# Kernel tuning notes

Hardware: AMD Instinct MI355X
Metric: run time of the kernel (lower is better)

The kernel has to match this reference:

```python
import jax, jax.numpy as jnp
import numpy as np

N, R, H, OUT = 512, 16, 16, 1
EPSILON = 1e-6
CUTOFF = 5.0  # ExpNormalSmearing cutoff_upper (cutoff_lower = 0)


def exp_normal_smearing(dist):
    # dist: (N, N, 1) -> (N, N, R); TorchMD-Net style ExpNormalSmearing
    start = jnp.exp(-CUTOFF)
    means = jnp.linspace(start, 1.0, R, dtype=dist.dtype)
    beta = (2.0 / R * (1.0 - start)) ** -2
    cutoff = 0.5 * (jnp.cos(dist * jnp.pi / CUTOFF) + 1.0) * (dist < CUTOFF)
    return cutoff * jnp.exp(-beta * (jnp.exp(-dist) - means) ** 2)


def setup_inputs() -> dict:
    key = jax.random.key(0)
    ks = jax.random.split(key, 9)
    s_in = 1.0 / np.sqrt(H * H)
    s_h = 1.0 / np.sqrt(H)
    return {
        "x": jax.random.normal(ks[0], (N, 3), jnp.float32) * 1.5,
        "W": jax.random.normal(ks[1], (2, N, R, H), jnp.float32) * 0.1,
        "W1": jax.random.normal(ks[2], (H, H * H), jnp.float32) * s_in,
        "b1": jax.random.normal(ks[3], (H,), jnp.float32) * 0.01,
        "W2": jax.random.normal(ks[4], (4 * R * H, H), jnp.float32) * s_h,
        "W3": jax.random.normal(ks[5], (H, H * H), jnp.float32) * s_in,
        "b3": jax.random.normal(ks[6], (H,), jnp.float32) * 0.01,
        "W4": jax.random.normal(ks[7], (OUT, H), jnp.float32) * s_h,
        "b4": jax.random.normal(ks[8], (OUT,), jnp.float32) * 0.01,
    }


def reference(x, W, W1, b1, W2, W3, b3, W4, b4):
    K, Q = W[0], W[1]                               # (N, R, H) each
    diff = x[:, None, :] - x[None, :, :]            # (N, N, 3)
    nsq = jnp.sum(diff * diff, axis=-1, keepdims=True) + EPSILON
    norm = jnp.sqrt(nsq)                            # (N, N, 1)
    diff = diff / nsq                               # note: divided by squared norm (faithful)
    sm = exp_normal_smearing(norm)                  # (N, N, R)
    basis = sm[..., None] * diff[..., None, :]      # (N, N, R, 3)

    bk = jnp.einsum('ijrb,jrc->icb', basis, K)      # (N, H, 3)
    bq = jnp.einsum('ijrb,jrc->icb', basis, Q)
    att = jnp.einsum('ihb,igb->ihg', bk, bq).reshape(N, H * H)
    att = jax.nn.silu(att @ W1.T + b1) @ W2.T       # (N, 4*R*H), second Linear bias-free

    left, right = att[:, : 2 * R * H], att[:, 2 * R * H:]
    pair = left[:, None, :] + right[None, :, :]     # (N, N, 2*R*H)
    K2 = pair[..., : R * H].reshape(N, N, R, H)
    Q2 = pair[..., R * H:].reshape(N, N, R, H)

    bk = jnp.einsum('ijrb,ijrc->icb', basis, K2)    # (N, H, 3)
    bq = jnp.einsum('ijrb,ijrc->icb', basis, Q2)
    att = jnp.einsum('ihb,igb->ihg', bk, bq).reshape(N, H * H)
    return jax.nn.silu(att @ W3.T + b3) @ W4.T + b4  # (N, OUT)
```

## Files before the change

### kernel.cpp

```cpp
#include <hip/hip_runtime.h>
#include <hip/hip_bf16.h>
#include <math.h>

#define NN 512

#define START 0.006737946999085467f
#define STEP  ((1.0f - START) * (1.0f/15.0f))
#define SB    (0.125f * (1.0f - START))
#define BETA  (1.0f/(SB*SB))
#define LOG2E 1.4426950408889634f
#define NB    (-(BETA)*LOG2E)


__global__ __launch_bounds__(256) void k1a(const float* __restrict__ x,
                                           const float* __restrict__ W,
                                           float* __restrict__ part1)
{
    const int ib = blockIdx.x & 127, jsH = blockIdx.x >> 7;
    const int i0 = ib * 4;
    const int tid = threadIdx.x;
    const int c = tid & 15, js = tid >> 4;
    const int lane = tid & 63, wv = tid >> 6;

    __shared__ float lG[1328];
    __shared__ float lP[256];
    __shared__ float s_part[4][16][26];

    const int gi = tid >> 6, gj = (tid >> 2) & 15, grq = tid & 3;
    const float gxi0 = x[(i0+gi)*3+0];
    const float gxi1 = x[(i0+gi)*3+1];
    const float gxi2 = x[(i0+gi)*3+2];

    float acc[24];
    #pragma unroll
    for (int v = 0; v < 24; ++v) acc[v] = 0.f;

    for (int jt = 0; jt < 4; ++jt) {
        const int jb = jsH*64 + jt*16;
        __syncthreads();

        {
            float d0 = gxi0 - x[(jb+gj)*3+0];
            float d1 = gxi1 - x[(jb+gj)*3+1];
            float d2 = gxi2 - x[(jb+gj)*3+2];
            float nsq = fmaf(d0,d0, fmaf(d1,d1, fmaf(d2,d2, 1e-6f)));
            float rs  = __builtin_amdgcn_rsqf(nsq);
            float nrm = nsq * rs;
            float inv = rs * rs;
            float cutv = 0.f;
            if (nrm < 5.0f) cutv = 0.5f*(__cosf(nrm*0.6283185307179586f)+1.0f);
            float en = exp2f(-LOG2E * nrm);
            if (grq == 0) {
                float4 dP; dP.x = d0*inv; dP.y = d1*inv; dP.z = d2*inv; dP.w = 0.f;
                *reinterpret_cast<float4*>(&lP[(gi*16+gj)*4]) = dP;
            }
            float4 g4;
            {
                float t0 = en - (START + STEP*(float)(grq*4+0));
                float t1 = en - (START + STEP*(float)(grq*4+1));
                float t2 = en - (START + STEP*(float)(grq*4+2));
                float t3 = en - (START + STEP*(float)(grq*4+3));
                g4.x = cutv * exp2f(NB*t0*t0);
                g4.y = cutv * exp2f(NB*t1*t1);
                g4.z = cutv * exp2f(NB*t2*t2);
                g4.w = cutv * exp2f(NB*t3*t3);
            }
            *reinterpret_cast<float4*>(&lG[gi*328 + gj*20 + grq*4]) = g4;
        }
        __syncthreads();

        const float* Kr = W + (size_t)(jb+js)*256 + c;
        const float* Qr = Kr + NN*256;
        float kk[16], qq[16];
        #pragma unroll
        for (int r = 0; r < 16; ++r) { kk[r] = Kr[r*16]; qq[r] = Qr[r*16]; }

        #pragma unroll
        for (int i = 0; i < 4; ++i) {
            const float4* gp = reinterpret_cast<const float4*>(&lG[i*328 + js*20]);
            float4 gA = gp[0], gB = gp[1], gC = gp[2], gD = gp[3];
            float tk = 0.f, tq = 0.f;
            tk = fmaf(gA.x,kk[ 0], tk); tq = fmaf(gA.x,qq[ 0], tq);
            tk = fmaf(gA.y,kk[ 1], tk); tq = fmaf(gA.y,qq[ 1], tq);
            tk = fmaf(gA.z,kk[ 2], tk); tq = fmaf(gA.z,qq[ 2], tq);
            tk = fmaf(gA.w,kk[ 3], tk); tq = fmaf(gA.w,qq[ 3], tq);
            tk = fmaf(gB.x,kk[ 4], tk); tq = fmaf(gB.x,qq[ 4], tq);
            tk = fmaf(gB.y,kk[ 5], tk); tq = fmaf(gB.y,qq[ 5], tq);
            tk = fmaf(gB.z,kk[ 6], tk); tq = fmaf(gB.z,qq[ 6], tq);
            tk = fmaf(gB.w,kk[ 7], tk); tq = fmaf(gB.w,qq[ 7], tq);
            tk = fmaf(gC.x,kk[ 8], tk); tq = fmaf(gC.x,qq[ 8], tq);
            tk = fmaf(gC.y,kk[ 9], tk); tq = fmaf(gC.y,qq[ 9], tq);
            tk = fmaf(gC.z,kk[10], tk); tq = fmaf(gC.z,qq[10], tq);
            tk = fmaf(gC.w,kk[11], tk); tq = fmaf(gC.w,qq[11], tq);
            tk = fmaf(gD.x,kk[12], tk); tq = fmaf(gD.x,qq[12], tq);
            tk = fmaf(gD.y,kk[13], tk); tq = fmaf(gD.y,qq[13], tq);
            tk = fmaf(gD.z,kk[14], tk); tq = fmaf(gD.z,qq[14], tq);
            tk = fmaf(gD.w,kk[15], tk); tq = fmaf(gD.w,qq[15], tq);
            float4 dd = *reinterpret_cast<const float4*>(&lP[(i*16+js)*4]);
            acc[i*6+0] = fmaf(tk, dd.x, acc[i*6+0]);
            acc[i*6+1] = fmaf(tk, dd.y, acc[i*6+1]);
            acc[i*6+2] = fmaf(tk, dd.z, acc[i*6+2]);
            acc[i*6+3] = fmaf(tq, dd.x, acc[i*6+3]);
            acc[i*6+4] = fmaf(tq, dd.y, acc[i*6+4]);
            acc[i*6+5] = fmaf(tq, dd.z, acc[i*6+5]);
        }
    }

    #pragma unroll
    for (int v = 0; v < 24; ++v) {
        float t = acc[v];
        t += __shfl_xor(t, 16);
        t += __shfl_xor(t, 32);
        if (lane < 16) s_part[wv][c][v] = t;
    }
    __syncthreads();

    for (int v = tid; v < 384; v += 256) {
        int i = v / 96, o = v - i*96;
        int kq = o / 48, rem = o - kq*48;
        int b = rem >> 4, c2 = rem & 15;
        int f = i*6 + kq*3 + b;
        float sum = s_part[0][c2][f] + s_part[1][c2][f]
                  + s_part[2][c2][f] + s_part[3][c2][f];
        part1[(i0+i)*768 + jsH*96 + o] = sum;
    }
}

__global__ __launch_bounds__(256) void k1b(const float* __restrict__ part1,
                                           const float* __restrict__ W1,
                                           const float* __restrict__ b1,
                                           const float* __restrict__ W2,
                                           float* __restrict__ att2)
{
    const int i = blockIdx.x;
    const int tid = threadIdx.x;
    __shared__ float s_bkq[96];
    __shared__ float s_att[256];
    __shared__ float s_z[16][16];
    __shared__ float s_a1[16];

    if (tid < 96) {
        const float* p = part1 + i*768 + tid;
        float s = 0.f;
        #pragma unroll
        for (int k = 0; k < 8; ++k) s += p[k*96];
        s_bkq[tid] = s;
    }
    __syncthreads();

    {
        int h = tid >> 4, g = tid & 15;
        s_att[tid] = s_bkq[     h]*s_bkq[48+     g]
                   + s_bkq[16 + h]*s_bkq[48+16 + g]
                   + s_bkq[32 + h]*s_bkq[48+32 + g];
    }
    __syncthreads();

    {
        int h = tid & 15, seg = tid >> 4;
        const float* w1 = W1 + h*256 + seg*16;
        const float* a  = s_att + seg*16;
        float p = 0.f;
        #pragma unroll
        for (int k = 0; k < 16; ++k) p = fmaf(a[k], w1[k], p);
        s_z[seg][h] = p;
    }
    __syncthreads();

    if (tid < 16) {
        float z = b1[tid];
        #pragma unroll
        for (int seg = 0; seg < 16; ++seg) z += s_z[seg][tid];
        s_a1[tid] = z / (1.0f + __expf(-z));
    }
    __syncthreads();

    float a1[16];
    #pragma unroll
    for (int cc = 0; cc < 16; ++cc) a1[cc] = s_a1[cc];
    #pragma unroll
    for (int p = 0; p < 4; ++p) {
        int o = tid + p*256;
        const float4* w2 = reinterpret_cast<const float4*>(W2 + o*16);
        float4 wa = w2[0], wb = w2[1], wc = w2[2], wd = w2[3];
        float accv = wa.x*a1[0] + wa.y*a1[1] + wa.z*a1[2] + wa.w*a1[3]
                   + wb.x*a1[4] + wb.y*a1[5] + wb.z*a1[6] + wb.w*a1[7]
                   + wc.x*a1[8] + wc.y*a1[9] + wc.z*a1[10]+ wc.w*a1[11]
                   + wd.x*a1[12]+ wd.y*a1[13]+ wd.z*a1[14]+ wd.w*a1[15];
        att2[i*1024 + o] = accv;
    }
}

__global__ __launch_bounds__(256) void k2a(const float* __restrict__ x,
                                           const float* __restrict__ att2,
                                           float* __restrict__ part2)
{
    const int ib = blockIdx.x & 127, jsH = blockIdx.x >> 7;
    const int i0 = ib * 4;
    const int tid = threadIdx.x;
    const int c = tid & 15, js = tid >> 4;
    const int lane = tid & 63, wv = tid >> 6;

    __shared__ float lG[1328];
    __shared__ float lP[256];
    __shared__ float s_part[4][16][38];

    const int gi = tid >> 6, gj = (tid >> 2) & 15, grq = tid & 3;
    const float gxi0 = x[(i0+gi)*3+0];
    const float gxi1 = x[(i0+gi)*3+1];
    const float gxi2 = x[(i0+gi)*3+2];

    float acc[36];
    #pragma unroll
    for (int v = 0; v < 36; ++v) acc[v] = 0.f;

    for (int jt = 0; jt < 4; ++jt) {
        const int jb = jsH*64 + jt*16;
        __syncthreads();

        {
            float d0 = gxi0 - x[(jb+gj)*3+0];
            float d1 = gxi1 - x[(jb+gj)*3+1];
            float d2 = gxi2 - x[(jb+gj)*3+2];
            float nsq = fmaf(d0,d0, fmaf(d1,d1, fmaf(d2,d2, 1e-6f)));
            float rs  = __builtin_amdgcn_rsqf(nsq);
            float nrm = nsq * rs;
            float inv = rs * rs;
            float cutv = 0.f;
            if (nrm < 5.0f) cutv = 0.5f*(__cosf(nrm*0.6283185307179586f)+1.0f);
            float en = exp2f(-LOG2E * nrm);
            if (grq == 0) {
                float4 dP; dP.x = d0*inv; dP.y = d1*inv; dP.z = d2*inv; dP.w = 0.f;
                *reinterpret_cast<float4*>(&lP[(gi*16+gj)*4]) = dP;
            }
            float4 g4;
            {
                float t0 = en - (START + STEP*(float)(grq*4+0));
                float t1 = en - (START + STEP*(float)(grq*4+1));
                float t2 = en - (START + STEP*(float)(grq*4+2));
                float t3 = en - (START + STEP*(float)(grq*4+3));
                g4.x = cutv * exp2f(NB*t0*t0);
                g4.y = cutv * exp2f(NB*t1*t1);
                g4.z = cutv * exp2f(NB*t2*t2);
                g4.w = cutv * exp2f(NB*t3*t3);
            }
            *reinterpret_cast<float4*>(&lG[gi*328 + gj*20 + grq*4]) = g4;
        }
        __syncthreads();

        const float* Rk = att2 + (size_t)(jb+js)*1024 + 512 + c;
        const float* Rq = Rk + 256;
        float kk[16], qq[16];
        #pragma unroll
        for (int r = 0; r < 16; ++r) { kk[r] = Rk[r*16]; qq[r] = Rq[r*16]; }

        #pragma unroll
        for (int i = 0; i < 4; ++i) {
            const float4* gp = reinterpret_cast<const float4*>(&lG[i*328 + js*20]);
            float4 gA = gp[0], gB = gp[1], gC = gp[2], gD = gp[3];
            float tk = 0.f, tq = 0.f;
            tk = fmaf(gA.x,kk[ 0], tk); tq = fmaf(gA.x,qq[ 0], tq);
            tk = fmaf(gA.y,kk[ 1], tk); tq = fmaf(gA.y,qq[ 1], tq);
            tk = fmaf(gA.z,kk[ 2], tk); tq = fmaf(gA.z,qq[ 2], tq);
            tk = fmaf(gA.w,kk[ 3], tk); tq = fmaf(gA.w,qq[ 3], tq);
            tk = fmaf(gB.x,kk[ 4], tk); tq = fmaf(gB.x,qq[ 4], tq);
            tk = fmaf(gB.y,kk[ 5], tk); tq = fmaf(gB.y,qq[ 5], tq);
            tk = fmaf(gB.z,kk[ 6], tk); tq = fmaf(gB.z,qq[ 6], tq);
            tk = fmaf(gB.w,kk[ 7], tk); tq = fmaf(gB.w,qq[ 7], tq);
            tk = fmaf(gC.x,kk[ 8], tk); tq = fmaf(gC.x,qq[ 8], tq);
            tk = fmaf(gC.y,kk[ 9], tk); tq = fmaf(gC.y,qq[ 9], tq);
            tk = fmaf(gC.z,kk[10], tk); tq = fmaf(gC.z,qq[10], tq);
            tk = fmaf(gC.w,kk[11], tk); tq = fmaf(gC.w,qq[11], tq);
            tk = fmaf(gD.x,kk[12], tk); tq = fmaf(gD.x,qq[12], tq);
            tk = fmaf(gD.y,kk[13], tk); tq = fmaf(gD.y,qq[13], tq);
            tk = fmaf(gD.z,kk[14], tk); tq = fmaf(gD.z,qq[14], tq);
            tk = fmaf(gD.w,kk[15], tk); tq = fmaf(gD.w,qq[15], tq);
            float4 dd = *reinterpret_cast<const float4*>(&lP[(i*16+js)*4]);
            acc[i*6+0] = fmaf(tk, dd.x, acc[i*6+0]);
            acc[i*6+1] = fmaf(tk, dd.y, acc[i*6+1]);
            acc[i*6+2] = fmaf(tk, dd.z, acc[i*6+2]);
            acc[i*6+3] = fmaf(tq, dd.x, acc[i*6+3]);
            acc[i*6+4] = fmaf(tq, dd.y, acc[i*6+4]);
            acc[i*6+5] = fmaf(tq, dd.z, acc[i*6+5]);
            float gc = lG[i*328 + js*20 + c];
            acc[24+i*3+0] = fmaf(gc, dd.x, acc[24+i*3+0]);
            acc[24+i*3+1] = fmaf(gc, dd.y, acc[24+i*3+1]);
            acc[24+i*3+2] = fmaf(gc, dd.z, acc[24+i*3+2]);
        }
    }

    #pragma unroll
    for (int v = 0; v < 36; ++v) {
        float t = acc[v];
        t += __shfl_xor(t, 16);
        t += __shfl_xor(t, 32);
        if (lane < 16) s_part[wv][c][v] = t;
    }
    __syncthreads();

    for (int v = tid; v < 576; v += 256) {
        int i = v / 144, o = v - i*144;
        int c2, f;
        if (o < 96) {
            int kq = o / 48, rem = o - kq*48;
            int b = rem >> 4; c2 = rem & 15;
            f = i*6 + kq*3 + b;
        } else {
            int oS = o - 96;
            int r = oS / 3, b = oS - r*3;
            c2 = r;
            f = 24 + i*3 + b;
        }
        float sum = s_part[0][c2][f] + s_part[1][c2][f]
                  + s_part[2][c2][f] + s_part[3][c2][f];
        part2[(i0+i)*1152 + jsH*144 + o] = sum;
    }
}

__global__ __launch_bounds__(256) void k2b(const float* __restrict__ att2,
                                           const float* __restrict__ part2,
                                           const float* __restrict__ W3,
                                           const float* __restrict__ b3,
                                           const float* __restrict__ W4,
                                           const float* __restrict__ b4,
                                           float* __restrict__ out)
{
    const int i = blockIdx.x;
    const int tid = threadIdx.x;
    __shared__ float s_red[144];
    __shared__ float s_att[256];
    __shared__ float s_z[16][16];
    __shared__ float s_a1[16];

    if (tid < 144) {
        const float* p = part2 + i*1152 + tid;
        float s = 0.f;
        #pragma unroll
        for (int k = 0; k < 8; ++k) s += p[k*144];
        s_red[tid] = s;
    }
    __syncthreads();

    if (tid < 96) {
        int kq = tid / 48, rem = tid - kq*48;
        int b = rem >> 4, c = rem & 15;
        const float* lrow = att2 + i*1024 + kq*256 + c;
        float add = 0.f;
        #pragma unroll
        for (int r = 0; r < 16; ++r)
            add = fmaf(lrow[r*16], s_red[96 + r*3 + b], add);
        s_red[tid] += add;
    }
    __syncthreads();

    {
        int h = tid >> 4, g = tid & 15;
        s_att[tid] = s_red[     h]*s_red[48+     g]
                   + s_red[16 + h]*s_red[48+16 + g]
                   + s_red[32 + h]*s_red[48+32 + g];
    }
    __syncthreads();

    {
        int h = tid & 15, seg = tid >> 4;
        const float* w3 = W3 + h*256 + seg*16;
        const float* a  = s_att + seg*16;
        float p = 0.f;
        #pragma unroll
        for (int k = 0; k < 16; ++k) p = fmaf(a[k], w3[k], p);
        s_z[seg][h] = p;
    }
    __syncthreads();

    if (tid < 16) {
        float z = b3[tid];
        #pragma unroll
        for (int seg = 0; seg < 16; ++seg) z += s_z[seg][tid];
        s_a1[tid] = z / (1.0f + __expf(-z));
    }
    __syncthreads();

    if (tid == 0) {
        float accv = b4[0];
        #pragma unroll
        for (int cc = 0; cc < 16; ++cc) accv = fmaf(s_a1[cc], W4[cc], accv);
        out[i] = accv;
    }
}

extern "C" void kernel_launch(void* const* d_in, const int* in_sizes, int n_in,
                              void* d_out, int out_size, void* d_ws, size_t ws_size,
                              hipStream_t stream) {
    (void)in_sizes; (void)n_in; (void)out_size; (void)ws_size;
    const float* x  = (const float*)d_in[0];
    const float* W  = (const float*)d_in[1];
    const float* W1 = (const float*)d_in[2];
    const float* b1 = (const float*)d_in[3];
    const float* W2 = (const float*)d_in[4];
    const float* W3 = (const float*)d_in[5];
    const float* b3 = (const float*)d_in[6];
    const float* W4 = (const float*)d_in[7];
    const float* b4 = (const float*)d_in[8];

    float* att2  = (float*)d_ws;
    float* part1 = att2 + 512*1024;
    float* part2 = part1 + 512*768;
    float* out   = (float*)d_out;

    k1a<<<1024, 256, 0, stream>>>(x, W, part1);
    k1b<<<512, 256, 0, stream>>>(part1, W1, b1, W2, att2);
    k2a<<<1024, 256, 0, stream>>>(x, att2, part2);
    k2b<<<512, 256, 0, stream>>>(att2, part2, W3, b3, W4, b4, out);
}
```

Before: 126.0 us.

## Fuse pairwise reduction with per-row MLP into one block per row

Merges each pairwise-reduction kernel with its follow-up MLP kernel. Each block now owns one row i and loops over all 512 j, so the partial-sum workspace and its global round trip go away and the launch count drops from four to two. In exchange, the reuse of loaded K/Q weights across four rows per block is lost, so each block reloads the full weight stream for a single row, which raises global/L2 traffic per output. The serial j loop is also longer, 32 iterations with two barriers each.

```diff
diff --git a/kernel.cpp b/kernel.cpp
--- a/kernel.cpp
+++ b/kernel.cpp
@@ -12,37 +12,44 @@
 #define NB    (-(BETA)*LOG2E)
 
 
-__global__ __launch_bounds__(256) void k1a(const float* __restrict__ x,
-                                           const float* __restrict__ W,
-                                           float* __restrict__ part1)
+__global__ __launch_bounds__(256) void k1(const float* __restrict__ x,
+                                          const float* __restrict__ W,
+                                          const float* __restrict__ W1,
+                                          const float* __restrict__ b1,
+                                          const float* __restrict__ W2,
+                                          float* __restrict__ att2)
 {
-    const int ib = blockIdx.x & 127, jsH = blockIdx.x >> 7;
-    const int i0 = ib * 4;
+    const int i   = blockIdx.x;
     const int tid = threadIdx.x;
-    const int c = tid & 15, js = tid >> 4;
+    const int c   = tid & 15, js = tid >> 4;
     const int lane = tid & 63, wv = tid >> 6;
 
-    __shared__ float lG[1328];
-    __shared__ float lP[256];
-    __shared__ float s_part[4][16][26];
-
-    const int gi = tid >> 6, gj = (tid >> 2) & 15, grq = tid & 3;
-    const float gxi0 = x[(i0+gi)*3+0];
-    const float gxi1 = x[(i0+gi)*3+1];
-    const float gxi2 = x[(i0+gi)*3+2];
-
-    float acc[24];
-    #pragma unroll
-    for (int v = 0; v < 24; ++v) acc[v] = 0.f;
-
-    for (int jt = 0; jt < 4; ++jt) {
-        const int jb = jsH*64 + jt*16;
+    __shared__ float lG[320];
+    __shared__ float lP[64];
+    __shared__ float s_part[4][16][6];
+    __shared__ float s_bkq[96];
+    __shared__ float s_att[256];
+    __shared__ float s_z[16][16];
+    __shared__ float s_a1[16];
+
+    const float xi0 = x[i*3+0], xi1 = x[i*3+1], xi2 = x[i*3+2];
+
+    float acc[6] = {0.f,0.f,0.f,0.f,0.f,0.f};
+
+    for (int jt = 0; jt < 32; ++jt) {
+        const int jb = jt*16;
         __syncthreads();
 
+        const float* Kr = W + (size_t)(jb+js)*256 + c;
+        const float* Qr = Kr + NN*256;
+        float kk[16], qq[16];
+        #pragma unroll
+        for (int r = 0; r < 16; ++r) { kk[r] = Kr[r*16]; qq[r] = Qr[r*16]; }
+
         {
-            float d0 = gxi0 - x[(jb+gj)*3+0];
-            float d1 = gxi1 - x[(jb+gj)*3+1];
-            float d2 = gxi2 - x[(jb+gj)*3+2];
+            float d0 = xi0 - x[(jb+c)*3+0];
+            float d1 = xi1 - x[(jb+c)*3+1];
+            float d2 = xi2 - x[(jb+c)*3+2];
             float nsq = fmaf(d0,d0, fmaf(d1,d1, fmaf(d2,d2, 1e-6f)));
             float rs  = __builtin_amdgcn_rsqf(nsq);
             float nrm = nsq * rs;
@@ -50,64 +57,45 @@
             float cutv = 0.f;
             if (nrm < 5.0f) cutv = 0.5f*(__cosf(nrm*0.6283185307179586f)+1.0f);
             float en = exp2f(-LOG2E * nrm);
-            if (grq == 0) {
+            if (js == 0) {
                 float4 dP; dP.x = d0*inv; dP.y = d1*inv; dP.z = d2*inv; dP.w = 0.f;
-                *reinterpret_cast<float4*>(&lP[(gi*16+gj)*4]) = dP;
+                *reinterpret_cast<float4*>(&lP[c*4]) = dP;
             }
-            float4 g4;
-            {
-                float t0 = en - (START + STEP*(float)(grq*4+0));
-                float t1 = en - (START + STEP*(float)(grq*4+1));
-                float t2 = en - (START + STEP*(float)(grq*4+2));
-                float t3 = en - (START + STEP*(float)(grq*4+3));
-                g4.x = cutv * exp2f(NB*t0*t0);
-                g4.y = cutv * exp2f(NB*t1*t1);
-                g4.z = cutv * exp2f(NB*t2*t2);
-                g4.w = cutv * exp2f(NB*t3*t3);
-            }
-            *reinterpret_cast<float4*>(&lG[gi*328 + gj*20 + grq*4]) = g4;
+            float t = en - (START + STEP*(float)js);
+            lG[c*20 + js] = cutv * exp2f(NB*t*t);
         }
         __syncthreads();
 
-        const float* Kr = W + (size_t)(jb+js)*256 + c;
-        const float* Qr = Kr + NN*256;
-        float kk[16], qq[16];
-        #pragma unroll
-        for (int r = 0; r < 16; ++r) { kk[r] = Kr[r*16]; qq[r] = Qr[r*16]; }
-
-        #pragma unroll
-        for (int i = 0; i < 4; ++i) {
-            const float4* gp = reinterpret_cast<const float4*>(&lG[i*328 + js*20]);
-            float4 gA = gp[0], gB = gp[1], gC = gp[2], gD = gp[3];
-            float tk = 0.f, tq = 0.f;
-            tk = fmaf(gA.x,kk[ 0], tk); tq = fmaf(gA.x,qq[ 0], tq);
-            tk = fmaf(gA.y,kk[ 1], tk); tq = fmaf(gA.y,qq[ 1], tq);
-            tk = fmaf(gA.z,kk[ 2], tk); tq = fmaf(gA.z,qq[ 2], tq);
-            tk = fmaf(gA.w,kk[ 3], tk); tq = fmaf(gA.w,qq[ 3], tq);
-            tk = fmaf(gB.x,kk[ 4], tk); tq = fmaf(gB.x,qq[ 4], tq);
-            tk = fmaf(gB.y,kk[ 5], tk); tq = fmaf(gB.y,qq[ 5], tq);
-            tk = fmaf(gB.z,kk[ 6], tk); tq = fmaf(gB.z,qq[ 6], tq);
-            tk = fmaf(gB.w,kk[ 7], tk); tq = fmaf(gB.w,qq[ 7], tq);
-            tk = fmaf(gC.x,kk[ 8], tk); tq = fmaf(gC.x,qq[ 8], tq);
-            tk = fmaf(gC.y,kk[ 9], tk); tq = fmaf(gC.y,qq[ 9], tq);
-            tk = fmaf(gC.z,kk[10], tk); tq = fmaf(gC.z,qq[10], tq);
-            tk = fmaf(gC.w,kk[11], tk); tq = fmaf(gC.w,qq[11], tq);
-            tk = fmaf(gD.x,kk[12], tk); tq = fmaf(gD.x,qq[12], tq);
-            tk = fmaf(gD.y,kk[13], tk); tq = fmaf(gD.y,qq[13], tq);
-            tk = fmaf(gD.z,kk[14], tk); tq = fmaf(gD.z,qq[14], tq);
-            tk = fmaf(gD.w,kk[15], tk); tq = fmaf(gD.w,qq[15], tq);
-            float4 dd = *reinterpret_cast<const float4*>(&lP[(i*16+js)*4]);
-            acc[i*6+0] = fmaf(tk, dd.x, acc[i*6+0]);
-            acc[i*6+1] = fmaf(tk, dd.y, acc[i*6+1]);
-            acc[i*6+2] = fmaf(tk, dd.z, acc[i*6+2]);
-            acc[i*6+3] = fmaf(tq, dd.x, acc[i*6+3]);
-            acc[i*6+4] = fmaf(tq, dd.y, acc[i*6+4]);
-            acc[i*6+5] = fmaf(tq, dd.z, acc[i*6+5]);
-        }
+        const float4* gp = reinterpret_cast<const float4*>(&lG[js*20]);
+        float4 gA = gp[0], gB = gp[1], gC = gp[2], gD = gp[3];
+        float tk = 0.f, tq = 0.f;
+        tk = fmaf(gA.x,kk[ 0], tk); tq = fmaf(gA.x,qq[ 0], tq);
+        tk = fmaf(gA.y,kk[ 1], tk); tq = fmaf(gA.y,qq[ 1], tq);
+        tk = fmaf(gA.z,kk[ 2], tk); tq = fmaf(gA.z,qq[ 2], tq);
+        tk = fmaf(gA.w,kk[ 3], tk); tq = fmaf(gA.w,qq[ 3], tq);
+        tk = fmaf(gB.x,kk[ 4], tk); tq = fmaf(gB.x,qq[ 4], tq);
+        tk = fmaf(gB.y,kk[ 5], tk); tq = fmaf(gB.y,qq[ 5], tq);
+        tk = fmaf(gB.z,kk[ 6], tk); tq = fmaf(gB.z,qq[ 6], tq);
+        tk = fmaf(gB.w,kk[ 7], tk); tq = fmaf(gB.w,qq[ 7], tq);
+        tk = fmaf(gC.x,kk[ 8], tk); tq = fmaf(gC.x,qq[ 8], tq);
+        tk = fmaf(gC.y,kk[ 9], tk); tq = fmaf(gC.y,qq[ 9], tq);
+        tk = fmaf(gC.z,kk[10], tk); tq = fmaf(gC.z,qq[10], tq);
+        tk = fmaf(gC.w,kk[11], tk); tq = fmaf(gC.w,qq[11], tq);
+        tk = fmaf(gD.x,kk[12], tk); tq = fmaf(gD.x,qq[12], tq);
+        tk = fmaf(gD.y,kk[13], tk); tq = fmaf(gD.y,qq[13], tq);
+        tk = fmaf(gD.z,kk[14], tk); tq = fmaf(gD.z,qq[14], tq);
+        tk = fmaf(gD.w,kk[15], tk); tq = fmaf(gD.w,qq[15], tq);
+        float4 dd = *reinterpret_cast<const float4*>(&lP[js*4]);
+        acc[0] = fmaf(tk, dd.x, acc[0]);
+        acc[1] = fmaf(tk, dd.y, acc[1]);
+        acc[2] = fmaf(tk, dd.z, acc[2]);
+        acc[3] = fmaf(tq, dd.x, acc[3]);
+        acc[4] = fmaf(tq, dd.y, acc[4]);
+        acc[5] = fmaf(tq, dd.z, acc[5]);
     }
 
     #pragma unroll
-    for (int v = 0; v < 24; ++v) {
+    for (int v = 0; v < 6; ++v) {
         float t = acc[v];
         t += __shfl_xor(t, 16);
         t += __shfl_xor(t, 32);
@@ -115,36 +103,12 @@
     }
     __syncthreads();
 
-    for (int v = tid; v < 384; v += 256) {
-        int i = v / 96, o = v - i*96;
-        int kq = o / 48, rem = o - kq*48;
+    if (tid < 96) {
+        int kq = tid / 48, rem = tid - kq*48;
         int b = rem >> 4, c2 = rem & 15;
-        int f = i*6 + kq*3 + b;
-        float sum = s_part[0][c2][f] + s_part[1][c2][f]
-                  + s_part[2][c2][f] + s_part[3][c2][f];
-        part1[(i0+i)*768 + jsH*96 + o] = sum;
-    }
-}
-
-__global__ __launch_bounds__(256) void k1b(const float* __restrict__ part1,
-                                           const float* __restrict__ W1,
-                                           const float* __restrict__ b1,
-                                           const float* __restrict__ W2,
-                                           float* __restrict__ att2)
-{
-    const int i = blockIdx.x;
-    const int tid = threadIdx.x;
-    __shared__ float s_bkq[96];
-    __shared__ float s_att[256];
-    __shared__ float s_z[16][16];
-    __shared__ float s_a1[16];
-
-    if (tid < 96) {
-        const float* p = part1 + i*768 + tid;
-        float s = 0.f;
-        #pragma unroll
-        for (int k = 0; k < 8; ++k) s += p[k*96];
-        s_bkq[tid] = s;
+        int f = kq*3 + b;
+        s_bkq[tid] = s_part[0][c2][f] + s_part[1][c2][f]
+                   + s_part[2][c2][f] + s_part[3][c2][f];
     }
     __syncthreads();
 
@@ -191,37 +155,45 @@
     }
 }
 
-__global__ __launch_bounds__(256) void k2a(const float* __restrict__ x,
-                                           const float* __restrict__ att2,
-                                           float* __restrict__ part2)
+__global__ __launch_bounds__(256) void k2(const float* __restrict__ x,
+                                          const float* __restrict__ att2,
+                                          const float* __restrict__ W3,
+                                          const float* __restrict__ b3,
+                                          const float* __restrict__ W4,
+                                          const float* __restrict__ b4,
+                                          float* __restrict__ out)
 {
-    const int ib = blockIdx.x & 127, jsH = blockIdx.x >> 7;
-    const int i0 = ib * 4;
+    const int i   = blockIdx.x;
     const int tid = threadIdx.x;
-    const int c = tid & 15, js = tid >> 4;
+    const int c   = tid & 15, js = tid >> 4;
     const int lane = tid & 63, wv = tid >> 6;
 
-    __shared__ float lG[1328];
-    __shared__ float lP[256];
-    __shared__ float s_part[4][16][38];
-
-    const int gi = tid >> 6, gj = (tid >> 2) & 15, grq = tid & 3;
-    const float gxi0 = x[(i0+gi)*3+0];
-    const float gxi1 = x[(i0+gi)*3+1];
-    const float gxi2 = x[(i0+gi)*3+2];
-
-    float acc[36];
-    #pragma unroll
-    for (int v = 0; v < 36; ++v) acc[v] = 0.f;
-
-    for (int jt = 0; jt < 4; ++jt) {
-        const int jb = jsH*64 + jt*16;
+    __shared__ float lG[320];
+    __shared__ float lP[64];
+    __shared__ float s_part[4][16][9];
+    __shared__ float s_red[144];
+    __shared__ float s_att[256];
+    __shared__ float s_z[16][16];
+    __shared__ float s_a1[16];
+
+    const float xi0 = x[i*3+0], xi1 = x[i*3+1], xi2 = x[i*3+2];
+
+    float acc[9] = {0.f,0.f,0.f,0.f,0.f,0.f,0.f,0.f,0.f};
+
+    for (int jt = 0; jt < 32; ++jt) {
+        const int jb = jt*16;
         __syncthreads();
 
+        const float* Rk = att2 + (size_t)(jb+js)*1024 + 512 + c;
+        const float* Rq = Rk + 256;
+        float kk[16], qq[16];
+        #pragma unroll
+        for (int r = 0; r < 16; ++r) { kk[r] = Rk[r*16]; qq[r] = Rq[r*16]; }
+
         {
-            float d0 = gxi0 - x[(jb+gj)*3+0];
-            float d1 = gxi1 - x[(jb+gj)*3+1];
-            float d2 = gxi2 - x[(jb+gj)*3+2];
+            float d0 = xi0 - x[(jb+c)*3+0];
+            float d1 = xi1 - x[(jb+c)*3+1];
+            float d2 = xi2 - x[(jb+c)*3+2];
             float nsq = fmaf(d0,d0, fmaf(d1,d1, fmaf(d2,d2, 1e-6f)));
             float rs  = __builtin_amdgcn_rsqf(nsq);
             float nrm = nsq * rs;
@@ -229,68 +201,49 @@
             float cutv = 0.f;
             if (nrm < 5.0f) cutv = 0.5f*(__cosf(nrm*0.6283185307179586f)+1.0f);
             float en = exp2f(-LOG2E * nrm);
-            if (grq == 0) {
+            if (js == 0) {
                 float4 dP; dP.x = d0*inv; dP.y = d1*inv; dP.z = d2*inv; dP.w = 0.f;
-                *reinterpret_cast<float4*>(&lP[(gi*16+gj)*4]) = dP;
+                *reinterpret_cast<float4*>(&lP[c*4]) = dP;
             }
-            float4 g4;
-            {
-                float t0 = en - (START + STEP*(float)(grq*4+0));
-                float t1 = en - (START + STEP*(float)(grq*4+1));
-                float t2 = en - (START + STEP*(float)(grq*4+2));
-                float t3 = en - (START + STEP*(float)(grq*4+3));
-                g4.x = cutv * exp2f(NB*t0*t0);
-                g4.y = cutv * exp2f(NB*t1*t1);
-                g4.z = cutv * exp2f(NB*t2*t2);
-                g4.w = cutv * exp2f(NB*t3*t3);
-            }
-            *reinterpret_cast<float4*>(&lG[gi*328 + gj*20 + grq*4]) = g4;
+            float t = en - (START + STEP*(float)js);
+            lG[c*20 + js] = cutv * exp2f(NB*t*t);
         }
         __syncthreads();
 
-        const float* Rk = att2 + (size_t)(jb+js)*1024 + 512 + c;
-        const float* Rq = Rk + 256;
-        float kk[16], qq[16];
-        #pragma unroll
-        for (int r = 0; r < 16; ++r) { kk[r] = Rk[r*16]; qq[r] = Rq[r*16]; }
-
-        #pragma unroll
-        for (int i = 0; i < 4; ++i) {
-            const float4* gp = reinterpret_cast<const float4*>(&lG[i*328 + js*20]);
-            float4 gA = gp[0], gB = gp[1], gC = gp[2], gD = gp[3];
-            float tk = 0.f, tq = 0.f;
-            tk = fmaf(gA.x,kk[ 0], tk); tq = fmaf(gA.x,qq[ 0], tq);
-            tk = fmaf(gA.y,kk[ 1], tk); tq = fmaf(gA.y,qq[ 1], tq);
-            tk = fmaf(gA.z,kk[ 2], tk); tq = fmaf(gA.z,qq[ 2], tq);
-            tk = fmaf(gA.w,kk[ 3], tk); tq = fmaf(gA.w,qq[ 3], tq);
-            tk = fmaf(gB.x,kk[ 4], tk); tq = fmaf(gB.x,qq[ 4], tq);
-            tk = fmaf(gB.y,kk[ 5], tk); tq = fmaf(gB.y,qq[ 5], tq);
-            tk = fmaf(gB.z,kk[ 6], tk); tq = fmaf(gB.z,qq[ 6], tq);
-            tk = fmaf(gB.w,kk[ 7], tk); tq = fmaf(gB.w,qq[ 7], tq);
-            tk = fmaf(gC.x,kk[ 8], tk); tq = fmaf(gC.x,qq[ 8], tq);
-            tk = fmaf(gC.y,kk[ 9], tk); tq = fmaf(gC.y,qq[ 9], tq);
-            tk = fmaf(gC.z,kk[10], tk); tq = fmaf(gC.z,qq[10], tq);
-            tk = fmaf(gC.w,kk[11], tk); tq = fmaf(gC.w,qq[11], tq);
-            tk = fmaf(gD.x,kk[12], tk); tq = fmaf(gD.x,qq[12], tq);
-            tk = fmaf(gD.y,kk[13], tk); tq = fmaf(gD.y,qq[13], tq);
-            tk = fmaf(gD.z,kk[14], tk); tq = fmaf(gD.z,qq[14], tq);
-            tk = fmaf(gD.w,kk[15], tk); tq = fmaf(gD.w,qq[15], tq);
-            float4 dd = *reinterpret_cast<const float4*>(&lP[(i*16+js)*4]);
-            acc[i*6+0] = fmaf(tk, dd.x, acc[i*6+0]);
-            acc[i*6+1] = fmaf(tk, dd.y, acc[i*6+1]);
-            acc[i*6+2] = fmaf(tk, dd.z, acc[i*6+2]);
-            acc[i*6+3] = fmaf(tq, dd.x, acc[i*6+3]);
-            acc[i*6+4] = fmaf(tq, dd.y, acc[i*6+4]);
-            acc[i*6+5] = fmaf(tq, dd.z, acc[i*6+5]);
-            float gc = lG[i*328 + js*20 + c];
-            acc[24+i*3+0] = fmaf(gc, dd.x, acc[24+i*3+0]);
-            acc[24+i*3+1] = fmaf(gc, dd.y, acc[24+i*3+1]);
-            acc[24+i*3+2] = fmaf(gc, dd.z, acc[24+i*3+2]);
-        }
+        const float4* gp = reinterpret_cast<const float4*>(&lG[js*20]);
+        float4 gA = gp[0], gB = gp[1], gC = gp[2], gD = gp[3];
+        float tk = 0.f, tq = 0.f;
+        tk = fmaf(gA.x,kk[ 0], tk); tq = fmaf(gA.x,qq[ 0], tq);
+        tk = fmaf(gA.y,kk[ 1], tk); tq = fmaf(gA.y,qq[ 1], tq);
+        tk = fmaf(gA.z,kk[ 2], tk); tq = fmaf(gA.z,qq[ 2], tq);
+        tk = fmaf(gA.w,kk[ 3], tk); tq = fmaf(gA.w,qq[ 3], tq);
+        tk = fmaf(gB.x,kk[ 4], tk); tq = fmaf(gB.x,qq[ 4], tq);
+        tk = fmaf(gB.y,kk[ 5], tk); tq = fmaf(gB.y,qq[ 5], tq);
+        tk = fmaf(gB.z,kk[ 6], tk); tq = fmaf(gB.z,qq[ 6], tq);
+        tk = fmaf(gB.w,kk[ 7], tk); tq = fmaf(gB.w,qq[ 7], tq);
+        tk = fmaf(gC.x,kk[ 8], tk); tq = fmaf(gC.x,qq[ 8], tq);
+        tk = fmaf(gC.y,kk[ 9], tk); tq = fmaf(gC.y,qq[ 9], tq);
+        tk = fmaf(gC.z,kk[10], tk); tq = fmaf(gC.z,qq[10], tq);
+        tk = fmaf(gC.w,kk[11], tk); tq = fmaf(gC.w,qq[11], tq);
+        tk = fmaf(gD.x,kk[12], tk); tq = fmaf(gD.x,qq[12], tq);
+        tk = fmaf(gD.y,kk[13], tk); tq = fmaf(gD.y,qq[13], tq);
+        tk = fmaf(gD.z,kk[14], tk); tq = fmaf(gD.z,qq[14], tq);
+        tk = fmaf(gD.w,kk[15], tk); tq = fmaf(gD.w,qq[15], tq);
+        float4 dd = *reinterpret_cast<const float4*>(&lP[js*4]);
+        acc[0] = fmaf(tk, dd.x, acc[0]);
+        acc[1] = fmaf(tk, dd.y, acc[1]);
+        acc[2] = fmaf(tk, dd.z, acc[2]);
+        acc[3] = fmaf(tq, dd.x, acc[3]);
+        acc[4] = fmaf(tq, dd.y, acc[4]);
+        acc[5] = fmaf(tq, dd.z, acc[5]);
+        float gc = lG[js*20 + c];
+        acc[6] = fmaf(gc, dd.x, acc[6]);
+        acc[7] = fmaf(gc, dd.y, acc[7]);
+        acc[8] = fmaf(gc, dd.z, acc[8]);
     }
 
     #pragma unroll
-    for (int v = 0; v < 36; ++v) {
+    for (int v = 0; v < 9; ++v) {
         float t = acc[v];
         t += __shfl_xor(t, 16);
         t += __shfl_xor(t, 32);
@@ -298,53 +251,30 @@
     }
     __syncthreads();
 
-    for (int v = tid; v < 576; v += 256) {
-        int i = v / 144, o = v - i*144;
-        int c2, f;
+    if (tid < 144) {
+        int o = tid;
+        float s;
         if (o < 96) {
             int kq = o / 48, rem = o - kq*48;
-            int b = rem >> 4; c2 = rem & 15;
-            f = i*6 + kq*3 + b;
+            int b = rem >> 4, c2 = rem & 15;
+            int f = kq*3 + b;
+            s = s_part[0][c2][f] + s_part[1][c2][f]
+              + s_part[2][c2][f] + s_part[3][c2][f];
         } else {
             int oS = o - 96;
             int r = oS / 3, b = oS - r*3;
-            c2 = r;
-            f = 24 + i*3 + b;
+            int f = 6 + b;
+            s = s_part[0][r][f] + s_part[1][r][f]
+              + s_part[2][r][f] + s_part[3][r][f];
         }
-        float sum = s_part[0][c2][f] + s_part[1][c2][f]
-                  + s_part[2][c2][f] + s_part[3][c2][f];
-        part2[(i0+i)*1152 + jsH*144 + o] = sum;
-    }
-}
-
-__global__ __launch_bounds__(256) void k2b(const float* __restrict__ att2,
-                                           const float* __restrict__ part2,
-                                           const float* __restrict__ W3,
-                                           const float* __restrict__ b3,
-                                           const float* __restrict__ W4,
-                                           const float* __restrict__ b4,
-                                           float* __restrict__ out)
-{
-    const int i = blockIdx.x;
-    const int tid = threadIdx.x;
-    __shared__ float s_red[144];
-    __shared__ float s_att[256];
-    __shared__ float s_z[16][16];
-    __shared__ float s_a1[16];
-
-    if (tid < 144) {
-        const float* p = part2 + i*1152 + tid;
-        float s = 0.f;
-        #pragma unroll
-        for (int k = 0; k < 8; ++k) s += p[k*144];
-        s_red[tid] = s;
+        s_red[o] = s;
     }
     __syncthreads();
 
     if (tid < 96) {
         int kq = tid / 48, rem = tid - kq*48;
-        int b = rem >> 4, c = rem & 15;
-        const float* lrow = att2 + i*1024 + kq*256 + c;
+        int b = rem >> 4, cc = rem & 15;
+        const float* lrow = att2 + i*1024 + kq*256 + cc;
         float add = 0.f;
         #pragma unroll
         for (int r = 0; r < 16; ++r)
@@ -402,13 +332,9 @@
     const float* W4 = (const float*)d_in[7];
     const float* b4 = (const float*)d_in[8];
 
-    float* att2  = (float*)d_ws;
-    float* part1 = att2 + 512*1024;
-    float* part2 = part1 + 512*768;
-    float* out   = (float*)d_out;
-
-    k1a<<<1024, 256, 0, stream>>>(x, W, part1);
-    k1b<<<512, 256, 0, stream>>>(part1, W1, b1, W2, att2);
-    k2a<<<1024, 256, 0, stream>>>(x, att2, part2);
-    k2b<<<512, 256, 0, stream>>>(att2, part2, W3, b3, W4, b4, out);
+    float* att2 = (float*)d_ws;
+    float* out  = (float*)d_out;
+
+    k1<<<512, 256, 0, stream>>>(x, W, W1, b1, W2, att2);
+    k2<<<512, 256, 0, stream>>>(x, att2, W3, b3, W4, b4, out);
 }
```

Measured after the change: 132.0 us. 1.05x slower.
